# Kernel tuning notes

Measured on AMD Instinct MI355X. Metric: run time of the kernel, lower is better.

## Reference

```python
import jax, jax.numpy as jnp
import numpy as np

IN_F = 4096
OUT_F = 11008
GROUPSIZE = 128
N_GROUPS = IN_F // GROUPSIZE  # 32


def setup_inputs() -> dict:
    key = jax.random.key(0)
    k1, k2, k3, k4 = jax.random.split(key, 4)
    x = jax.random.normal(k1, (4, 2048, IN_F), dtype=jnp.float32)
    # packed 4-bit weights: 8 nibbles per int32 along the input dim
    qweight = jax.random.randint(k2, (IN_F // 8, OUT_F), 0, 2**31 - 1, dtype=jnp.int32)
    # packed 4-bit zero points: 8 nibbles per int32 along the output dim
    qzeros = jax.random.randint(k3, (N_GROUPS, OUT_F // 8), 0, 2**31 - 1, dtype=jnp.int32)
    scales = jax.random.uniform(k4, (N_GROUPS, OUT_F), dtype=jnp.float32,
                                minval=0.001, maxval=0.01)
    g_idx = (jnp.arange(IN_F, dtype=jnp.int32) // GROUPSIZE).astype(jnp.int32)
    return {"x": x, "qweight": qweight, "scales": scales,
            "qzeros": qzeros, "g_idx": g_idx}


def _dequantize(qweight, scales, qzeros, g_idx):
    """GPTQ v2 dequant: W[i, j] = scales[g_idx[i], j] * (q[i, j] - (z[g_idx[i], j] + 1))."""
    shifts = jnp.arange(8, dtype=jnp.int32) * 4  # nibble shift amounts
    # unpack weights along input dim: [in/8, 8, out] -> [in, out]
    q = (qweight[:, None, :] >> shifts[None, :, None]) & 0xF
    q = q.reshape(-1, qweight.shape[1]).astype(scales.dtype)
    # unpack zeros along output dim: [g, out/8, 8] -> [g, out]; +1 per GPTQ v2
    z = ((qzeros[:, :, None] >> shifts[None, None, :]) & 0xF) + 1
    z = z.reshape(qzeros.shape[0], -1).astype(scales.dtype)
    return scales[g_idx] * (q - z[g_idx])  # [in, out]


def reference(x, qweight, scales, qzeros, g_idx):
    W = _dequantize(qweight, scales, qzeros, g_idx)  # [IN_F, OUT_F]
    return jnp.einsum('bsi,io->bso', x, W)
```

## Files before the change

### kernel.cpp

```cpp
#include <hip/hip_runtime.h>
#include <hip/hip_bf16.h>

#define IN_F 4096
#define OUT_F 11008

typedef __bf16 bf16_t;
typedef bf16_t bf16x8 __attribute__((ext_vector_type(8)));
typedef float f32x4 __attribute__((ext_vector_type(4)));
typedef unsigned int u32;

__global__ __launch_bounds__(256) void cvt_x_kernel(const float* __restrict__ x,
                                                    bf16_t* __restrict__ xb) {
    size_t i = ((size_t)blockIdx.x * 256 + threadIdx.x) * 8;
    f32x4 v0 = __builtin_nontemporal_load((const f32x4*)(x + i));
    f32x4 v1 = __builtin_nontemporal_load((const f32x4*)(x + i + 4));
    bf16x8 h;
    h[0]=(bf16_t)v0[0]; h[1]=(bf16_t)v0[1]; h[2]=(bf16_t)v0[2]; h[3]=(bf16_t)v0[3];
    h[4]=(bf16_t)v1[0]; h[5]=(bf16_t)v1[1]; h[6]=(bf16_t)v1[2]; h[7]=(bf16_t)v1[3];
    *(bf16x8*)(xb + i) = h;
}

__global__ __launch_bounds__(256) void dequant_kernel(const int* __restrict__ qweight,
                                                      const float* __restrict__ scales,
                                                      const int* __restrict__ qzeros,
                                                      bf16_t* __restrict__ wt) {
    const int n   = blockIdx.x * 256 + threadIdx.x;
    const int kw0 = blockIdx.y * 4;
    const int g   = kw0 >> 4;
    const float s  = scales[(size_t)g * OUT_F + n];
    const int   zw = qzeros[(size_t)g * (OUT_F / 8) + (n >> 3)];
    const float nsz = -s * (float)(((zw >> ((n & 7) * 4)) & 0xF) + 1);
    bf16_t* dst = wt + (size_t)n * IN_F + kw0 * 8;
    #pragma unroll
    for (int j = 0; j < 4; ++j) {
        const int w = __builtin_nontemporal_load(&qweight[(size_t)(kw0 + j) * OUT_F + n]);
        bf16x8 h;
        #pragma unroll
        for (int b = 0; b < 8; ++b)
            h[b] = (bf16_t)fmaf((float)((w >> (4 * b)) & 0xF), s, nsz);
        *(bf16x8*)(dst + j * 8) = h;
    }
}


#define NI (IN_F / 128)

__global__ __launch_bounds__(512, 2) void gemm_8ph(const bf16_t* __restrict__ A,
                                                   const bf16_t* __restrict__ B,
                                                   float* __restrict__ C) {
    __shared__ __align__(16) bf16_t smemA[2 * 2 * 128 * 64];
    __shared__ __align__(16) bf16_t smemB[2 * 2 * 128 * 64];

    const int tid  = threadIdx.x;
    const int lane = tid & 63;
    const int wid  = tid >> 6;
    const int wr   = wid >> 2;
    const int wc   = wid & 3;

    const int bid = blockIdx.x;
    const int swz = (bid & 7) * 172 + (bid >> 3);
    const int bx = swz % 43;
    const int by = swz / 43;
    const int m0 = by * 256;
    const int n0 = bx * 256;

    int lr0, kb0, lr1, kb1;
    {
        int L0 = tid * 16;
        int p0 = L0 ^ (((L0 >> 7) & 7) << 4);
        lr0 = p0 >> 7; kb0 = (p0 & 127) >> 1;
        int L1 = (512 + tid) * 16;
        int p1 = L1 ^ (((L1 >> 7) & 7) << 4);
        lr1 = p1 >> 7; kb1 = (p1 & 127) >> 1;
    }

    const int xm = (lane & 7) << 4;
    const int arow = lane & 15;
    int colk[2];
    #pragma unroll
    for (int ks = 0; ks < 2; ++ks)
        colk[ks] = ((ks * 64) + ((lane >> 4) * 16)) ^ xm;

#define STAGE(smem, buf, half, src, rbase, koff)                                           \
    do {                                                                                   \
        const bf16_t* g0_ = (src) + (size_t)((rbase) + lr0) * IN_F + (koff) + kb0;         \
        __builtin_amdgcn_global_load_lds(                                                  \
            (const __attribute__((address_space(1))) u32*)g0_,                             \
            (__attribute__((address_space(3))) u32*)((char*)(smem) + (buf) * 32768 +       \
                                                     (half) * 16384 + wid * 1024),         \
            16, 0, 0);                                                                     \
        const bf16_t* g1_ = (src) + (size_t)((rbase) + lr1) * IN_F + (koff) + kb1;         \
        __builtin_amdgcn_global_load_lds(                                                  \
            (const __attribute__((address_space(1))) u32*)g1_,                             \
            (__attribute__((address_space(3))) u32*)((char*)(smem) + (buf) * 32768 +       \
                                                     (half) * 16384 + 8192 + wid * 1024),  \
            16, 0, 0);                                                                     \
    } while (0)

#define STAGE_A(buf, half, koff) STAGE(smemA, buf, half, A, m0 + (half) * 128, koff)
#define STAGE_B(buf, half, koff) STAGE(smemB, buf, half, B, n0 + (half) * 128, koff)

#define LOAD_A_FRAGS(dst, buf, mbase)                                                      \
    _Pragma("unroll") for (int mm = 0; mm < 4; ++mm)                                       \
    _Pragma("unroll") for (int ks = 0; ks < 2; ++ks)                                       \
        dst[mm * 2 + ks] = *(const bf16x8*)((const char*)smemA + (buf) * 32768 +           \
            wr * 16384 + (((mbase) + mm) * 16 + arow) * 128 + colk[ks]);

#define LOAD_B_PAIR(dst, buf, P)                                                           \
    _Pragma("unroll") for (int nn = 0; nn < 2; ++nn)                                       \
    _Pragma("unroll") for (int ks = 0; ks < 2; ++ks)                                       \
        dst[nn * 2 + ks] = *(const bf16x8*)((const char*)smemB + (buf) * 32768 +           \
            (wc >> 1) * 16384 + ((wc & 1) * 64 + ((P) * 2 + nn) * 16 + arow) * 128 +       \
            colk[ks]);

#define MFMA_Q(aArr, bArr, mbase, nbase)                                                   \
    __builtin_amdgcn_s_setprio(1);                                                         \
    _Pragma("unroll") for (int mm = 0; mm < 4; ++mm)                                       \
    _Pragma("unroll") for (int nn = 0; nn < 2; ++nn)                                       \
    _Pragma("unroll") for (int ks = 0; ks < 2; ++ks)                                       \
        acc[(mbase) + mm][(nbase) + nn] = __builtin_amdgcn_mfma_f32_16x16x32_bf16(         \
            aArr[mm * 2 + ks], bArr[nn * 2 + ks], acc[(mbase) + mm][(nbase) + nn],         \
            0, 0, 0);                                                                      \
    __builtin_amdgcn_s_setprio(0);

#define BAR() __builtin_amdgcn_s_barrier()
#define VMCNT6() asm volatile("s_waitcnt vmcnt(6)" ::: "memory")
#define VMCNT4() asm volatile("s_waitcnt vmcnt(4)" ::: "memory")
#define VMCNT0() asm volatile("s_waitcnt vmcnt(0)" ::: "memory")

    f32x4 acc[8][4];
    #pragma unroll
    for (int m = 0; m < 8; ++m)
        #pragma unroll
        for (int n = 0; n < 4; ++n)
            acc[m][n] = (f32x4)0.0f;

    bf16x8 aR[8], b01[4], b23[4];

    STAGE_A(0, 0, 0);  STAGE_A(0, 1, 0);
    STAGE_B(0, 0, 0);  STAGE_B(0, 1, 0);
    STAGE_B(1, 0, 64); STAGE_B(1, 1, 64);
    STAGE_A(1, 0, 64);
    VMCNT6();
    BAR();

    for (int i = 0; i < NI; ++i) {
        const int  kc = i * 128;
        const int  kn = kc + 128;
        const bool nl = (i + 1 < NI);

        LOAD_A_FRAGS(aR, 0, 0);
        LOAD_B_PAIR(b01, 0, 0);
        STAGE_A(1, 1, kc + 64);
        MFMA_Q(aR, b01, 0, 0);
        BAR();
        LOAD_B_PAIR(b23, 0, 1);
        MFMA_Q(aR, b23, 0, 2);
        BAR();
        LOAD_A_FRAGS(aR, 0, 4);
        if (nl) STAGE_B(0, 0, kn);
        MFMA_Q(aR, b01, 4, 0);
        BAR();
        if (nl) STAGE_A(0, 0, kn);
        MFMA_Q(aR, b23, 4, 2);
        if (nl) VMCNT4(); else VMCNT0();
        BAR();
        LOAD_A_FRAGS(aR, 1, 0);
        LOAD_B_PAIR(b01, 1, 0);
        if (nl) STAGE_A(0, 1, kn);
        MFMA_Q(aR, b01, 0, 0);
        BAR();
        LOAD_B_PAIR(b23, 1, 1);
        if (nl) STAGE_B(0, 1, kn);
        MFMA_Q(aR, b23, 0, 2);
        BAR();
        LOAD_A_FRAGS(aR, 1, 4);
        if (nl) STAGE_B(1, 0, kn + 64);
        MFMA_Q(aR, b01, 4, 0);
        BAR();
        if (nl) { STAGE_B(1, 1, kn + 64); STAGE_A(1, 0, kn + 64); }
        MFMA_Q(aR, b23, 4, 2);
        if (nl) VMCNT6();
        BAR();
    }

    const int cn  = lane & 15;
    const int cr4 = (lane >> 4) * 4;
    #pragma unroll
    for (int m = 0; m < 8; ++m) {
        #pragma unroll
        for (int r = 0; r < 4; ++r) {
            const int grow = m0 + wr * 128 + m * 16 + cr4 + r;
            float* orow = C + (size_t)grow * OUT_F + n0 + wc * 64 + cn;
            #pragma unroll
            for (int n = 0; n < 4; ++n)
                __builtin_nontemporal_store(acc[m][n][r], orow + n * 16);
        }
    }
}

#define BMf 128
#define BNf 128
#define BKf 32
#define LDPF 40

__global__ __launch_bounds__(256, 2) void gptq_gemm_fused(
    const float* __restrict__ x, const int* __restrict__ qweight,
    const float* __restrict__ scales, const int* __restrict__ qzeros,
    float* __restrict__ out)
{
    __shared__ bf16_t As[BMf * LDPF];
    __shared__ bf16_t Bs[BNf * LDPF];
    const int tid = threadIdx.x, lane = tid & 63, wid = tid >> 6;
    const int wr = wid >> 1, wc = wid & 1;
    const int m0 = blockIdx.y * BMf, n0 = blockIdx.x * BNf;
    const int a_row = tid >> 2, a_slot = tid & 3;
    const int b_k8l = tid >> 7, b_n = tid & 127;

    f32x4 acc[4][4];
    #pragma unroll
    for (int i = 0; i < 4; ++i)
        #pragma unroll
        for (int j = 0; j < 4; ++j) acc[i][j] = (f32x4)0.0f;

    for (int kt = 0; kt < IN_F / BKf; ++kt) {
        const int k0 = kt * BKf;
        const int g  = k0 >> 7;
        __syncthreads();
        #pragma unroll
        for (int p = 0; p < 2; ++p) {
            const int row = a_row + p * 64;
            const float* src = x + (size_t)(m0 + row) * IN_F + k0 + a_slot * 8;
            f32x4 v0 = *(const f32x4*)src;
            f32x4 v1 = *(const f32x4*)(src + 4);
            bf16x8 h;
            h[0]=(bf16_t)v0[0]; h[1]=(bf16_t)v0[1]; h[2]=(bf16_t)v0[2]; h[3]=(bf16_t)v0[3];
            h[4]=(bf16_t)v1[0]; h[5]=(bf16_t)v1[1]; h[6]=(bf16_t)v1[2]; h[7]=(bf16_t)v1[3];
            *(bf16x8*)(&As[row * LDPF + a_slot * 8]) = h;
        }
        {
            const int gn = n0 + b_n;
            const float s  = scales[(size_t)g * OUT_F + gn];
            const int   zw = qzeros[(size_t)g * (OUT_F / 8) + (gn >> 3)];
            const float sz = s * (float)(((zw >> ((gn & 7) * 4)) & 0xF) + 1);
            #pragma unroll
            for (int p = 0; p < 2; ++p) {
                const int k8l = b_k8l + p * 2;
                const int w = qweight[(size_t)(k0 / 8 + k8l) * OUT_F + gn];
                bf16x8 h;
                #pragma unroll
                for (int j = 0; j < 8; ++j)
                    h[j] = (bf16_t)fmaf((float)((w >> (4 * j)) & 0xF), s, -sz);
                *(bf16x8*)(&Bs[b_n * LDPF + k8l * 8]) = h;
            }
        }
        __syncthreads();
        bf16x8 af[4], bfr[4];
        #pragma unroll
        for (int m = 0; m < 4; ++m)
            af[m] = *(const bf16x8*)(&As[(wr * 64 + m * 16 + (lane & 15)) * LDPF + (lane >> 4) * 8]);
        #pragma unroll
        for (int n = 0; n < 4; ++n)
            bfr[n] = *(const bf16x8*)(&Bs[(wc * 64 + n * 16 + (lane & 15)) * LDPF + (lane >> 4) * 8]);
        #pragma unroll
        for (int m = 0; m < 4; ++m)
            #pragma unroll
            for (int n = 0; n < 4; ++n)
                acc[m][n] = __builtin_amdgcn_mfma_f32_16x16x32_bf16(af[m], bfr[n], acc[m][n], 0, 0, 0);
    }
    const int cn = lane & 15, cr4 = (lane >> 4) * 4;
    #pragma unroll
    for (int m = 0; m < 4; ++m)
        #pragma unroll
        for (int r = 0; r < 4; ++r) {
            const int grow = m0 + wr * 64 + m * 16 + cr4 + r;
            float* orow = out + (size_t)grow * OUT_F + n0 + wc * 64 + cn;
            #pragma unroll
            for (int n = 0; n < 4; ++n) orow[n * 16] = acc[m][n][r];
        }
}

extern "C" void kernel_launch(void* const* d_in, const int* in_sizes, int n_in,
                              void* d_out, int out_size, void* d_ws, size_t ws_size,
                              hipStream_t stream) {
    const float* x       = (const float*)d_in[0];
    const int*   qweight = (const int*)d_in[1];
    const float* scales  = (const float*)d_in[2];
    const int*   qzeros  = (const int*)d_in[3];
    float* out = (float*)d_out;

    const int M = in_sizes[0] / IN_F;
    const size_t xb_bytes = (size_t)M * IN_F * 2;
    const size_t wt_bytes = (size_t)IN_F * OUT_F * 2;

    if (ws_size >= xb_bytes + wt_bytes && (M % 256) == 0) {
        bf16_t* xb = (bf16_t*)d_ws;
        bf16_t* wt = (bf16_t*)((char*)d_ws + xb_bytes);
        cvt_x_kernel<<<dim3((M * IN_F) / (256 * 8)), dim3(256), 0, stream>>>(x, xb);
        dequant_kernel<<<dim3(OUT_F / 256, IN_F / 32), dim3(256), 0, stream>>>(
            qweight, scales, qzeros, wt);
        const int nwg = (OUT_F / 256) * (M / 256);
        gemm_8ph<<<dim3(nwg), dim3(512), 0, stream>>>(xb, wt, out);
    } else {
        gptq_gemm_fused<<<dim3(OUT_F / BNf, M / BMf), dim3(256), 0, stream>>>(
            x, qweight, scales, qzeros, out);
    }
}
```

Before: 811.7 us.

## Restructure bf16 GEMM to 4 waves with 128x128 per-wave tiles and register double-buffering

```diff
diff --git a/kernel.cpp b/kernel.cpp
--- a/kernel.cpp
+++ b/kernel.cpp
@@ -45,17 +45,17 @@
 
 #define NI (IN_F / 128)
 
-__global__ __launch_bounds__(512, 2) void gemm_8ph(const bf16_t* __restrict__ A,
-                                                   const bf16_t* __restrict__ B,
-                                                   float* __restrict__ C) {
+__global__ __launch_bounds__(256, 1) void gemm_4w(const bf16_t* __restrict__ A,
+                                                  const bf16_t* __restrict__ B,
+                                                  float* __restrict__ C) {
     __shared__ __align__(16) bf16_t smemA[2 * 2 * 128 * 64];
     __shared__ __align__(16) bf16_t smemB[2 * 2 * 128 * 64];
 
     const int tid  = threadIdx.x;
     const int lane = tid & 63;
     const int wid  = tid >> 6;
-    const int wr   = wid >> 2;
-    const int wc   = wid & 3;
+    const int wr   = wid >> 1;
+    const int wc   = wid & 1;
 
     const int bid = blockIdx.x;
     const int swz = (bid & 7) * 172 + (bid >> 3);
@@ -64,14 +64,12 @@
     const int m0 = by * 256;
     const int n0 = bx * 256;
 
-    int lr0, kb0, lr1, kb1;
-    {
-        int L0 = tid * 16;
-        int p0 = L0 ^ (((L0 >> 7) & 7) << 4);
-        lr0 = p0 >> 7; kb0 = (p0 & 127) >> 1;
-        int L1 = (512 + tid) * 16;
-        int p1 = L1 ^ (((L1 >> 7) & 7) << 4);
-        lr1 = p1 >> 7; kb1 = (p1 & 127) >> 1;
+    int offg[4];
+    #pragma unroll
+    for (int j = 0; j < 4; ++j) {
+        int L = j * 4096 + tid * 16;
+        int p = L ^ (((L >> 7) & 7) << 4);
+        offg[j] = (p >> 7) * IN_F + ((p & 127) >> 1);
     }
 
     const int xm = (lane & 7) << 4;
@@ -81,106 +79,110 @@
     for (int ks = 0; ks < 2; ++ks)
         colk[ks] = ((ks * 64) + ((lane >> 4) * 16)) ^ xm;
 
-#define STAGE(smem, buf, half, src, rbase, koff)                                           \
-    do {                                                                                   \
-        const bf16_t* g0_ = (src) + (size_t)((rbase) + lr0) * IN_F + (koff) + kb0;         \
+    const bf16_t* gA = A + (size_t)m0 * IN_F;
+    const bf16_t* gB = B + (size_t)n0 * IN_F;
+
+#define STAGE_HALF(smem_, gbase_, buf, half, koff)                                         \
+    _Pragma("unroll") for (int j = 0; j < 4; ++j) {                                        \
         __builtin_amdgcn_global_load_lds(                                                  \
-            (const __attribute__((address_space(1))) u32*)g0_,                             \
-            (__attribute__((address_space(3))) u32*)((char*)(smem) + (buf) * 32768 +       \
-                                                     (half) * 16384 + wid * 1024),         \
+            (const __attribute__((address_space(1))) u32*)                                 \
+                ((gbase_) + (size_t)(half) * (128 * IN_F) + (koff) + offg[j]),             \
+            (__attribute__((address_space(3))) u32*)((char*)(smem_) + (buf) * 32768 +      \
+                (half) * 16384 + j * 4096 + wid * 1024),                                   \
             16, 0, 0);                                                                     \
-        const bf16_t* g1_ = (src) + (size_t)((rbase) + lr1) * IN_F + (koff) + kb1;         \
-        __builtin_amdgcn_global_load_lds(                                                  \
-            (const __attribute__((address_space(1))) u32*)g1_,                             \
-            (__attribute__((address_space(3))) u32*)((char*)(smem) + (buf) * 32768 +       \
-                                                     (half) * 16384 + 8192 + wid * 1024),  \
-            16, 0, 0);                                                                     \
-    } while (0)
-
-#define STAGE_A(buf, half, koff) STAGE(smemA, buf, half, A, m0 + (half) * 128, koff)
-#define STAGE_B(buf, half, koff) STAGE(smemB, buf, half, B, n0 + (half) * 128, koff)
-
-#define LOAD_A_FRAGS(dst, buf, mbase)                                                      \
-    _Pragma("unroll") for (int mm = 0; mm < 4; ++mm)                                       \
+    }
+
+#define RD_A2(dst, buf, mg)                                                                \
+    _Pragma("unroll") for (int mm = 0; mm < 2; ++mm)                                       \
     _Pragma("unroll") for (int ks = 0; ks < 2; ++ks)                                       \
-        dst[mm * 2 + ks] = *(const bf16x8*)((const char*)smemA + (buf) * 32768 +           \
-            wr * 16384 + (((mbase) + mm) * 16 + arow) * 128 + colk[ks]);
-
-#define LOAD_B_PAIR(dst, buf, P)                                                           \
+        dst[((mg) + mm) * 2 + ks] = *(const bf16x8*)((const char*)smemA + (buf) * 32768 +  \
+            wr * 16384 + (((mg) + mm) * 16 + arow) * 128 + colk[ks]);
+
+#define RD_B(dst, buf, np)                                                                 \
     _Pragma("unroll") for (int nn = 0; nn < 2; ++nn)                                       \
     _Pragma("unroll") for (int ks = 0; ks < 2; ++ks)                                       \
         dst[nn * 2 + ks] = *(const bf16x8*)((const char*)smemB + (buf) * 32768 +           \
-            (wc >> 1) * 16384 + ((wc & 1) * 64 + ((P) * 2 + nn) * 16 + arow) * 128 +       \
-            colk[ks]);
-
-#define MFMA_Q(aArr, bArr, mbase, nbase)                                                   \
-    __builtin_amdgcn_s_setprio(1);                                                         \
-    _Pragma("unroll") for (int mm = 0; mm < 4; ++mm)                                       \
+            wc * 16384 + ((np) * 32 + nn * 16 + arow) * 128 + colk[ks]);
+
+#define MFMA_P(aArr, bArr, np)                                                             \
+    _Pragma("unroll") for (int mm = 0; mm < 8; ++mm)                                       \
     _Pragma("unroll") for (int nn = 0; nn < 2; ++nn)                                       \
     _Pragma("unroll") for (int ks = 0; ks < 2; ++ks)                                       \
-        acc[(mbase) + mm][(nbase) + nn] = __builtin_amdgcn_mfma_f32_16x16x32_bf16(         \
-            aArr[mm * 2 + ks], bArr[nn * 2 + ks], acc[(mbase) + mm][(nbase) + nn],         \
-            0, 0, 0);                                                                      \
-    __builtin_amdgcn_s_setprio(0);
+        acc[mm][(np) * 2 + nn] = __builtin_amdgcn_mfma_f32_16x16x32_bf16(                  \
+            aArr[mm * 2 + ks], bArr[nn * 2 + ks], acc[mm][(np) * 2 + nn], 0, 0, 0);
 
 #define BAR() __builtin_amdgcn_s_barrier()
-#define VMCNT6() asm volatile("s_waitcnt vmcnt(6)" ::: "memory")
+#define VMCNT8() asm volatile("s_waitcnt vmcnt(8)" ::: "memory")
 #define VMCNT4() asm volatile("s_waitcnt vmcnt(4)" ::: "memory")
 #define VMCNT0() asm volatile("s_waitcnt vmcnt(0)" ::: "memory")
 
-    f32x4 acc[8][4];
+    f32x4 acc[8][8];
     #pragma unroll
     for (int m = 0; m < 8; ++m)
         #pragma unroll
-        for (int n = 0; n < 4; ++n)
+        for (int n = 0; n < 8; ++n)
             acc[m][n] = (f32x4)0.0f;
 
-    bf16x8 aR[8], b01[4], b23[4];
-
-    STAGE_A(0, 0, 0);  STAGE_A(0, 1, 0);
-    STAGE_B(0, 0, 0);  STAGE_B(0, 1, 0);
-    STAGE_B(1, 0, 64); STAGE_B(1, 1, 64);
-    STAGE_A(1, 0, 64);
-    VMCNT6();
+    bf16x8 aS0[16], aS1[16], bS0[4], bS1[4];
+
+    STAGE_HALF(smemA, gA, 0, 0, 0); STAGE_HALF(smemA, gA, 0, 1, 0);
+    STAGE_HALF(smemB, gB, 0, 0, 0); STAGE_HALF(smemB, gB, 0, 1, 0);
+    STAGE_HALF(smemA, gA, 1, 0, 64); STAGE_HALF(smemA, gA, 1, 1, 64);
+    STAGE_HALF(smemB, gB, 1, 0, 64); STAGE_HALF(smemB, gB, 1, 1, 64);
+    VMCNT8();
     BAR();
+    RD_A2(aS0, 0, 0); RD_A2(aS0, 0, 2); RD_A2(aS0, 0, 4); RD_A2(aS0, 0, 6);
+    RD_B(bS1, 0, 0);
 
     for (int i = 0; i < NI; ++i) {
-        const int  kc = i * 128;
-        const int  kn = kc + 128;
+        const int  kn = i * 128 + 128;
         const bool nl = (i + 1 < NI);
 
-        LOAD_A_FRAGS(aR, 0, 0);
-        LOAD_B_PAIR(b01, 0, 0);
-        STAGE_A(1, 1, kc + 64);
-        MFMA_Q(aR, b01, 0, 0);
-        BAR();
-        LOAD_B_PAIR(b23, 0, 1);
-        MFMA_Q(aR, b23, 0, 2);
-        BAR();
-        LOAD_A_FRAGS(aR, 0, 4);
-        if (nl) STAGE_B(0, 0, kn);
-        MFMA_Q(aR, b01, 4, 0);
-        BAR();
-        if (nl) STAGE_A(0, 0, kn);
-        MFMA_Q(aR, b23, 4, 2);
-        if (nl) VMCNT4(); else VMCNT0();
-        BAR();
-        LOAD_A_FRAGS(aR, 1, 0);
-        LOAD_B_PAIR(b01, 1, 0);
-        if (nl) STAGE_A(0, 1, kn);
-        MFMA_Q(aR, b01, 0, 0);
-        BAR();
-        LOAD_B_PAIR(b23, 1, 1);
-        if (nl) STAGE_B(0, 1, kn);
-        MFMA_Q(aR, b23, 0, 2);
-        BAR();
-        LOAD_A_FRAGS(aR, 1, 4);
-        if (nl) STAGE_B(1, 0, kn + 64);
-        MFMA_Q(aR, b01, 4, 0);
-        BAR();
-        if (nl) { STAGE_B(1, 1, kn + 64); STAGE_A(1, 0, kn + 64); }
-        MFMA_Q(aR, b23, 4, 2);
-        if (nl) VMCNT6();
+        RD_A2(aS1, 1, 0);
+        RD_B(bS0, 0, 1);
+        if (nl) STAGE_HALF(smemA, gA, 0, 0, kn);
+        MFMA_P(aS0, bS1, 0);
+        BAR();
+        RD_A2(aS1, 1, 2);
+        RD_B(bS1, 0, 2);
+        if (nl) STAGE_HALF(smemA, gA, 0, 1, kn);
+        MFMA_P(aS0, bS0, 1);
+        BAR();
+        RD_A2(aS1, 1, 4);
+        RD_B(bS0, 0, 3);
+        MFMA_P(aS0, bS1, 2);
+        if (nl) VMCNT8(); else VMCNT0();
+        BAR();
+        RD_A2(aS1, 1, 6);
+        RD_B(bS1, 1, 0);
+        if (nl) STAGE_HALF(smemB, gB, 0, 0, kn);
+        MFMA_P(aS0, bS0, 3);
+        if (nl) VMCNT4();
+        BAR();
+        if (nl) RD_A2(aS0, 0, 0);
+        RD_B(bS0, 1, 1);
+        if (nl) STAGE_HALF(smemB, gB, 0, 1, kn);
+        MFMA_P(aS1, bS1, 0);
+        BAR();
+        if (nl) RD_A2(aS0, 0, 2);
+        RD_B(bS1, 1, 2);
+        if (nl) STAGE_HALF(smemA, gA, 1, 0, kn + 64);
+        MFMA_P(aS1, bS0, 1);
+        BAR();
+        if (nl) RD_A2(aS0, 0, 4);
+        RD_B(bS0, 1, 3);
+        if (nl) STAGE_HALF(smemA, gA, 1, 1, kn + 64);
+        MFMA_P(aS1, bS1, 2);
+        if (nl) VMCNT8();
+        BAR();
+        if (nl) {
+            RD_A2(aS0, 0, 6);
+            RD_B(bS1, 0, 0);
+            STAGE_HALF(smemB, gB, 1, 0, kn + 64);
+            STAGE_HALF(smemB, gB, 1, 1, kn + 64);
+        }
+        MFMA_P(aS1, bS0, 3);
+        if (nl) VMCNT8();
         BAR();
     }
 
@@ -191,10 +193,10 @@
         #pragma unroll
         for (int r = 0; r < 4; ++r) {
             const int grow = m0 + wr * 128 + m * 16 + cr4 + r;
-            float* orow = C + (size_t)grow * OUT_F + n0 + wc * 64 + cn;
+            float* orow = C + (size_t)grow * OUT_F + n0 + wc * 128 + cn;
             #pragma unroll
-            for (int n = 0; n < 4; ++n)
-                __builtin_nontemporal_store(acc[m][n][r], orow + n * 16);
+            for (int n = 0; n < 8; ++n)
+                orow[n * 16] = acc[m][n][r];
         }
     }
 }
@@ -300,7 +302,7 @@
         dequant_kernel<<<dim3(OUT_F / 256, IN_F / 32), dim3(256), 0, stream>>>(
             qweight, scales, qzeros, wt);
         const int nwg = (OUT_F / 256) * (M / 256);
-        gemm_8ph<<<dim3(nwg), dim3(512), 0, stream>>>(xb, wt, out);
+        gemm_4w<<<dim3(nwg), dim3(256), 0, stream>>>(xb, wt, out);
     } else {
         gptq_gemm_fused<<<dim3(OUT_F / BNf, M / BMf), dim3(256), 0, stream>>>(
             x, qweight, scales, qzeros, out);
```

Result: slower. 1.008 ms (+24.2%).

## Fuse int4 dequantization into GEMM mainloop, loading packed weights to registers

Applied to the files above, without the earlier changes.

```diff
diff --git a/kernel.cpp b/kernel.cpp
--- a/kernel.cpp
+++ b/kernel.cpp
@@ -20,36 +20,15 @@
     *(bf16x8*)(xb + i) = h;
 }
 
-__global__ __launch_bounds__(256) void dequant_kernel(const int* __restrict__ qweight,
-                                                      const float* __restrict__ scales,
-                                                      const int* __restrict__ qzeros,
-                                                      bf16_t* __restrict__ wt) {
-    const int n   = blockIdx.x * 256 + threadIdx.x;
-    const int kw0 = blockIdx.y * 4;
-    const int g   = kw0 >> 4;
-    const float s  = scales[(size_t)g * OUT_F + n];
-    const int   zw = qzeros[(size_t)g * (OUT_F / 8) + (n >> 3)];
-    const float nsz = -s * (float)(((zw >> ((n & 7) * 4)) & 0xF) + 1);
-    bf16_t* dst = wt + (size_t)n * IN_F + kw0 * 8;
-    #pragma unroll
-    for (int j = 0; j < 4; ++j) {
-        const int w = __builtin_nontemporal_load(&qweight[(size_t)(kw0 + j) * OUT_F + n]);
-        bf16x8 h;
-        #pragma unroll
-        for (int b = 0; b < 8; ++b)
-            h[b] = (bf16_t)fmaf((float)((w >> (4 * b)) & 0xF), s, nsz);
-        *(bf16x8*)(dst + j * 8) = h;
-    }
-}
-
 
 #define NI (IN_F / 128)
 
-__global__ __launch_bounds__(512, 2) void gemm_8ph(const bf16_t* __restrict__ A,
-                                                   const bf16_t* __restrict__ B,
-                                                   float* __restrict__ C) {
+__global__ __launch_bounds__(512, 2) void gemm_dq(const bf16_t* __restrict__ A,
+                                                  const int* __restrict__ qweight,
+                                                  const float* __restrict__ scales,
+                                                  const int* __restrict__ qzeros,
+                                                  float* __restrict__ C) {
     __shared__ __align__(16) bf16_t smemA[2 * 2 * 128 * 64];
-    __shared__ __align__(16) bf16_t smemB[2 * 2 * 128 * 64];
 
     const int tid  = threadIdx.x;
     const int lane = tid & 63;
@@ -81,37 +60,50 @@
     for (int ks = 0; ks < 2; ++ks)
         colk[ks] = ((ks * 64) + ((lane >> 4) * 16)) ^ xm;
 
-#define STAGE(smem, buf, half, src, rbase, koff)                                           \
+    const int ncol = n0 + wc * 64 + (lane & 15);
+    const int* qwp = qweight + (size_t)(lane >> 4) * OUT_F + ncol;
+    const float* sp = scales + ncol;
+    const int*   zp = qzeros + (ncol >> 3);
+    const int    zsh = (lane & 7) * 4;
+
+#define STAGE_A(buf, half, koff)                                                           \
     do {                                                                                   \
-        const bf16_t* g0_ = (src) + (size_t)((rbase) + lr0) * IN_F + (koff) + kb0;         \
+        const bf16_t* g0_ = A + (size_t)(m0 + (half) * 128 + lr0) * IN_F + (koff) + kb0;   \
         __builtin_amdgcn_global_load_lds(                                                  \
             (const __attribute__((address_space(1))) u32*)g0_,                             \
-            (__attribute__((address_space(3))) u32*)((char*)(smem) + (buf) * 32768 +       \
+            (__attribute__((address_space(3))) u32*)((char*)smemA + (buf) * 32768 +        \
                                                      (half) * 16384 + wid * 1024),         \
             16, 0, 0);                                                                     \
-        const bf16_t* g1_ = (src) + (size_t)((rbase) + lr1) * IN_F + (koff) + kb1;         \
+        const bf16_t* g1_ = A + (size_t)(m0 + (half) * 128 + lr1) * IN_F + (koff) + kb1;   \
         __builtin_amdgcn_global_load_lds(                                                  \
             (const __attribute__((address_space(1))) u32*)g1_,                             \
-            (__attribute__((address_space(3))) u32*)((char*)(smem) + (buf) * 32768 +       \
+            (__attribute__((address_space(3))) u32*)((char*)smemA + (buf) * 32768 +        \
                                                      (half) * 16384 + 8192 + wid * 1024),  \
             16, 0, 0);                                                                     \
     } while (0)
 
-#define STAGE_A(buf, half, koff) STAGE(smemA, buf, half, A, m0 + (half) * 128, koff)
-#define STAGE_B(buf, half, koff) STAGE(smemB, buf, half, B, n0 + (half) * 128, koff)
-
-#define LOAD_A_FRAGS(dst, buf, mbase)                                                      \
+#define RD_A(dst, buf, mbase)                                                              \
     _Pragma("unroll") for (int mm = 0; mm < 4; ++mm)                                       \
     _Pragma("unroll") for (int ks = 0; ks < 2; ++ks)                                       \
         dst[mm * 2 + ks] = *(const bf16x8*)((const char*)smemA + (buf) * 32768 +           \
             wr * 16384 + (((mbase) + mm) * 16 + arow) * 128 + colk[ks]);
 
-#define LOAD_B_PAIR(dst, buf, P)                                                           \
+#define LOAD_W(dst, rowoff)                                                                \
+    _Pragma("unroll") for (int nt = 0; nt < 4; ++nt)                                       \
+    _Pragma("unroll") for (int ks = 0; ks < 2; ++ks)                                       \
+        dst[nt * 2 + ks] = qwp[(size_t)((rowoff) + ks * 4) * OUT_F + nt * 16];
+
+#define DEQ(dst, wArr, nt0)                                                                \
     _Pragma("unroll") for (int nn = 0; nn < 2; ++nn)                                       \
-    _Pragma("unroll") for (int ks = 0; ks < 2; ++ks)                                       \
-        dst[nn * 2 + ks] = *(const bf16x8*)((const char*)smemB + (buf) * 32768 +           \
-            (wc >> 1) * 16384 + ((wc & 1) * 64 + ((P) * 2 + nn) * 16 + arow) * 128 +       \
-            colk[ks]);
+    _Pragma("unroll") for (int ks = 0; ks < 2; ++ks) {                                     \
+        const int wv_ = wArr[((nt0) + nn) * 2 + ks];                                       \
+        const float s_ = s0[(nt0) + nn];                                                   \
+        const float z_ = nsz0[(nt0) + nn];                                                 \
+        bf16x8 h_;                                                                         \
+        _Pragma("unroll") for (int j = 0; j < 8; ++j)                                      \
+            h_[j] = (bf16_t)fmaf((float)((wv_ >> (4 * j)) & 0xF), s_, z_);                 \
+        dst[nn * 2 + ks] = h_;                                                             \
+    }
 
 #define MFMA_Q(aArr, bArr, mbase, nbase)                                                   \
     __builtin_amdgcn_s_setprio(1);                                                         \
@@ -124,8 +116,7 @@
     __builtin_amdgcn_s_setprio(0);
 
 #define BAR() __builtin_amdgcn_s_barrier()
-#define VMCNT6() asm volatile("s_waitcnt vmcnt(6)" ::: "memory")
-#define VMCNT4() asm volatile("s_waitcnt vmcnt(4)" ::: "memory")
+#define VMCNT2() asm volatile("s_waitcnt vmcnt(2)" ::: "memory")
 #define VMCNT0() asm volatile("s_waitcnt vmcnt(0)" ::: "memory")
 
     f32x4 acc[8][4];
@@ -136,12 +127,22 @@
             acc[m][n] = (f32x4)0.0f;
 
     bf16x8 aR[8], b01[4], b23[4];
-
-    STAGE_A(0, 0, 0);  STAGE_A(0, 1, 0);
-    STAGE_B(0, 0, 0);  STAGE_B(0, 1, 0);
-    STAGE_B(1, 0, 64); STAGE_B(1, 1, 64);
+    int   w0[8], w1[8];
+    float s0[4], nsz0[4];
+    float sraw[4]; int zraw[4];
+
+    LOAD_W(w0, 0);
+    #pragma unroll
+    for (int nt = 0; nt < 4; ++nt) { sraw[nt] = sp[nt * 16]; zraw[nt] = zp[nt * 2]; }
+    #pragma unroll
+    for (int nt = 0; nt < 4; ++nt) {
+        s0[nt] = sraw[nt];
+        nsz0[nt] = -sraw[nt] * (float)(((zraw[nt] >> zsh) & 0xF) + 1);
+    }
+    DEQ(b01, w0, 0);
+    STAGE_A(0, 0, 0); STAGE_A(0, 1, 0);
     STAGE_A(1, 0, 64);
-    VMCNT6();
+    VMCNT2();
     BAR();
 
     for (int i = 0; i < NI; ++i) {
@@ -149,39 +150,56 @@
         const int  kn = kc + 128;
         const bool nl = (i + 1 < NI);
 
-        LOAD_A_FRAGS(aR, 0, 0);
-        LOAD_B_PAIR(b01, 0, 0);
+        RD_A(aR, 0, 0);
         STAGE_A(1, 1, kc + 64);
+        DEQ(b23, w0, 2);
         MFMA_Q(aR, b01, 0, 0);
         BAR();
-        LOAD_B_PAIR(b23, 0, 1);
+        LOAD_W(w1, 8);
         MFMA_Q(aR, b23, 0, 2);
         BAR();
-        LOAD_A_FRAGS(aR, 0, 4);
-        if (nl) STAGE_B(0, 0, kn);
+        RD_A(aR, 0, 4);
         MFMA_Q(aR, b01, 4, 0);
         BAR();
         if (nl) STAGE_A(0, 0, kn);
+        DEQ(b01, w1, 0);
         MFMA_Q(aR, b23, 4, 2);
-        if (nl) VMCNT4(); else VMCNT0();
-        BAR();
-        LOAD_A_FRAGS(aR, 1, 0);
-        LOAD_B_PAIR(b01, 1, 0);
+        if (nl) VMCNT2(); else VMCNT0();
+        BAR();
+        RD_A(aR, 1, 0);
         if (nl) STAGE_A(0, 1, kn);
+        DEQ(b23, w1, 2);
         MFMA_Q(aR, b01, 0, 0);
         BAR();
-        LOAD_B_PAIR(b23, 1, 1);
-        if (nl) STAGE_B(0, 1, kn);
+        if (nl) {
+            LOAD_W(w0, 16);
+            #pragma unroll
+            for (int nt = 0; nt < 4; ++nt) {
+                sraw[nt] = sp[(size_t)(i + 1) * OUT_F + nt * 16];
+                zraw[nt] = zp[(size_t)(i + 1) * (OUT_F / 8) + nt * 2];
+            }
+        }
         MFMA_Q(aR, b23, 0, 2);
         BAR();
-        LOAD_A_FRAGS(aR, 1, 4);
-        if (nl) STAGE_B(1, 0, kn + 64);
+        RD_A(aR, 1, 4);
+        if (nl) {
+            #pragma unroll
+            for (int nt = 0; nt < 4; ++nt) {
+                s0[nt] = sraw[nt];
+                nsz0[nt] = -sraw[nt] * (float)(((zraw[nt] >> zsh) & 0xF) + 1);
+            }
+        }
         MFMA_Q(aR, b01, 4, 0);
         BAR();
-        if (nl) { STAGE_B(1, 1, kn + 64); STAGE_A(1, 0, kn + 64); }
+        if (nl) {
+            STAGE_A(1, 0, kn + 64);
+            DEQ(b01, w0, 0);
+        }
         MFMA_Q(aR, b23, 4, 2);
-        if (nl) VMCNT6();
-        BAR();
+        if (nl) VMCNT2();
+        BAR();
+
+        qwp += (size_t)16 * OUT_F;
     }
 
     const int cn  = lane & 15;
@@ -194,7 +212,7 @@
             float* orow = C + (size_t)grow * OUT_F + n0 + wc * 64 + cn;
             #pragma unroll
             for (int n = 0; n < 4; ++n)
-                __builtin_nontemporal_store(acc[m][n][r], orow + n * 16);
+                orow[n * 16] = acc[m][n][r];
         }
     }
 }
@@ -291,16 +309,12 @@
 
     const int M = in_sizes[0] / IN_F;
     const size_t xb_bytes = (size_t)M * IN_F * 2;
-    const size_t wt_bytes = (size_t)IN_F * OUT_F * 2;
-
-    if (ws_size >= xb_bytes + wt_bytes && (M % 256) == 0) {
+
+    if (ws_size >= xb_bytes && (M % 256) == 0) {
         bf16_t* xb = (bf16_t*)d_ws;
-        bf16_t* wt = (bf16_t*)((char*)d_ws + xb_bytes);
         cvt_x_kernel<<<dim3((M * IN_F) / (256 * 8)), dim3(256), 0, stream>>>(x, xb);
-        dequant_kernel<<<dim3(OUT_F / 256, IN_F / 32), dim3(256), 0, stream>>>(
-            qweight, scales, qzeros, wt);
         const int nwg = (OUT_F / 256) * (M / 256);
-        gemm_8ph<<<dim3(nwg), dim3(512), 0, stream>>>(xb, wt, out);
+        gemm_dq<<<dim3(nwg), dim3(512), 0, stream>>>(xb, qweight, scales, qzeros, out);
     } else {
         gptq_gemm_fused<<<dim3(OUT_F / BNf, M / BMf), dim3(256), 0, stream>>>(
             x, qweight, scales, qzeros, out);
```

After: 1.122 ms. +38.2%, slower.
